# Kernel optimization log

Measured on AMD Instinct MI355X. Metric: run time of the kernel, lower is better.

## Reference

```python
import jax, jax.numpy as jnp
import numpy as np

MODEL_DIM = 1024
EXPAND = 2
INNER = MODEL_DIM * EXPAND      # 2048
STATE = 16
K = 4                           # conv kernel
B, S = 2, 1024


def setup_inputs() -> dict:
    key = jax.random.key(0)
    ks = jax.random.split(key, 12)
    sd = 0.02
    hidden = jax.random.normal(ks[0], (B, S, MODEL_DIM), dtype=jnp.float32)
    w_in = jax.random.normal(ks[1], (2 * INNER, MODEL_DIM), dtype=jnp.float32) * sd
    w_conv = jax.random.normal(ks[2], (INNER, 1, K), dtype=jnp.float32) * 0.2   # depthwise [O, I/g=1, K]
    b_conv = jax.random.normal(ks[3], (INNER,), dtype=jnp.float32) * 0.02
    w_dt = jax.random.normal(ks[4], (INNER, INNER), dtype=jnp.float32) * sd
    b_dt = jnp.full((INNER,), -2.0, dtype=jnp.float32)  # small softplus(dt) at init
    w_b = jax.random.normal(ks[5], (INNER * STATE, INNER), dtype=jnp.float32) * sd
    w_c = jax.random.normal(ks[6], (INNER * STATE, INNER), dtype=jnp.float32) * sd
    w_out = jax.random.normal(ks[7], (MODEL_DIM, INNER), dtype=jnp.float32) * sd
    # a_log = log(arange(1, N+1)) repeated over inner_dim
    a_log = jnp.log(jnp.tile(jnp.arange(1, STATE + 1, dtype=jnp.float32), (INNER, 1)))
    d = jnp.ones((INNER,), dtype=jnp.float32)
    return {"hidden": hidden, "w_in": w_in, "w_conv": w_conv, "b_conv": b_conv,
            "w_dt": w_dt, "b_dt": b_dt, "w_b": w_b, "w_c": w_c, "w_out": w_out,
            "a_log": a_log, "d": d}


def reference(hidden, w_in, w_conv, b_conv, w_dt, b_dt, w_b, w_c, w_out, a_log, d):
    batch, seq_len, _ = hidden.shape
    inner, state_n = a_log.shape
    k = w_conv.shape[-1]

    proj = hidden @ w_in.T                     # [B,S,2*inner]
    u, gate = jnp.split(proj, 2, axis=-1)

    # depthwise causal conv: torch pads k-1 both sides then slices [:, :, :S]
    # which equals left-only padding of k-1
    x = u.transpose(0, 2, 1)                   # [B,inner,S]
    x = jax.lax.conv_general_dilated(
        x, w_conv, window_strides=(1,), padding=[(k - 1, 0)],
        dimension_numbers=("NCH", "OIH", "NCH"), feature_group_count=inner)
    u = jax.nn.silu(x.transpose(0, 2, 1) + b_conv)   # [B,S,inner]
    gate = jax.nn.sigmoid(gate)

    delta = jax.nn.softplus(u @ w_dt.T + b_dt)                       # [B,S,inner]
    bmat = (u @ w_b.T).reshape(batch, seq_len, inner, state_n)       # [B,S,inner,N]
    cmat = (u @ w_c.T).reshape(batch, seq_len, inner, state_n)
    a = -jnp.exp(a_log)                                              # [inner,N]

    def step(state, xs):
        d_t, u_t, b_t, c_t, g_t = xs
        state = jnp.exp(d_t[..., None] * a) * state + d_t[..., None] * b_t * u_t[..., None]
        y = jnp.sum(c_t * state, axis=-1) + d * u_t
        return state, y * g_t

    xs = (delta.transpose(1, 0, 2), u.transpose(1, 0, 2),
          bmat.transpose(1, 0, 2, 3), cmat.transpose(1, 0, 2, 3),
          gate.transpose(1, 0, 2))
    init = jnp.zeros((batch, inner, state_n), dtype=hidden.dtype)
    _, ys = jax.lax.scan(step, init, xs)       # ys: [S,B,inner]
    mixed = ys.transpose(1, 0, 2)              # [B,S,inner]
    return mixed @ w_out.T                     # dropout is identity in eval mode
```

## Files before the change

### kernel.cpp

```cpp
#include <hip/hip_runtime.h>
#include <hip/hip_bf16.h>

typedef __bf16 bf16_t;
typedef __bf16 bf16x8 __attribute__((ext_vector_type(8)));
typedef float f32x4 __attribute__((ext_vector_type(4)));

#define MODEL_DIM 1024
#define INNER 2048
#define STATE 16
#define BATCH 2
#define SEQ 1024
#define BS (BATCH * SEQ)
#define PROJ_N (2 * INNER)
#define BCN (INNER * STATE)
#define NCHUNK 64
#define CLEN (SEQ / NCHUNK)

__device__ __forceinline__ void load_lds_16B(const void* g, void* l) {
  __builtin_amdgcn_global_load_lds(
      (const __attribute__((address_space(1))) unsigned int*)g,
      (__attribute__((address_space(3))) unsigned int*)l,
      16, 0, 0);
}

__global__ void cast_f32_bf16(const float* __restrict__ in,
                              bf16_t* __restrict__ out, long n4) {
  long idx = (long)blockIdx.x * blockDim.x + threadIdx.x;
  long stride = (long)gridDim.x * blockDim.x;
  for (long i = idx; i < n4; i += stride) {
    float4 v = ((const float4*)in)[i];
    union { bf16_t b[4]; ushort4 u; } cv;
    cv.b[0] = (bf16_t)v.x; cv.b[1] = (bf16_t)v.y;
    cv.b[2] = (bf16_t)v.z; cv.b[3] = (bf16_t)v.w;
    ((ushort4*)out)[i] = cv.u;
  }
}

template <int EPI>
__global__ __launch_bounds__(256)
void gemm_bt(const bf16_t* __restrict__ A, const bf16_t* __restrict__ Bt,
             void* __restrict__ C, const float* __restrict__ bias,
             int nbx, int nby, int N, int K) {
  __shared__ bf16_t Ash[128 * 64];
  __shared__ bf16_t Bsh[128 * 64];
  const int tid = threadIdx.x;
  const int wave = tid >> 6, lane = tid & 63;

  const int bid = blockIdx.x;
  const int xcd = bid & 7, local = bid >> 3;
  const int bcol = (xcd * (nbx >> 3) + local / nby) * 128;
  const int brow = (local % nby) * 128;

  const int wr = wave >> 1, wc = wave & 1;

  f32x4 acc[4][4] = {};

  const int seg_base = wave * 4;
  const int lrow = lane >> 3;
  const int scol = ((lane & 7) ^ (lrow & 7)) * 8;
  const int r15 = lane & 15, g = lane >> 4, l7 = lane & 7;

  for (int k0 = 0; k0 < K; k0 += 64) {
#pragma unroll
    for (int c = 0; c < 4; ++c) {
      int seg = seg_base + c;
      int row = seg * 8 + lrow;
      const bf16_t* ga = A + (size_t)(brow + row) * K + k0 + scol;
      load_lds_16B(ga, (void*)(Ash + seg * 512));
      const bf16_t* gb = Bt + (size_t)(bcol + row) * K + k0 + scol;
      load_lds_16B(gb, (void*)(Bsh + seg * 512));
    }
    asm volatile("s_waitcnt vmcnt(0)");
    __syncthreads();

#pragma unroll
    for (int ks = 0; ks < 2; ++ks) {
      bf16x8 af[4], bfr[4];
#pragma unroll
      for (int t = 0; t < 4; ++t) {
        int arow = wr * 64 + t * 16 + r15;
        int brw  = wc * 64 + t * 16 + r15;
        int slot = ((ks * 4 + g) ^ l7) * 8;
        af[t]  = *(const bf16x8*)&Ash[arow * 64 + slot];
        bfr[t] = *(const bf16x8*)&Bsh[brw * 64 + slot];
      }
#pragma unroll
      for (int mt = 0; mt < 4; ++mt)
#pragma unroll
        for (int nt = 0; nt < 4; ++nt)
          acc[mt][nt] = __builtin_amdgcn_mfma_f32_16x16x32_bf16(
              af[mt], bfr[nt], acc[mt][nt], 0, 0, 0);
    }
    __syncthreads();
  }

#pragma unroll
  for (int mt = 0; mt < 4; ++mt) {
#pragma unroll
    for (int nt = 0; nt < 4; ++nt) {
      int col = bcol + wc * 64 + nt * 16 + r15;
#pragma unroll
      for (int j = 0; j < 4; ++j) {
        int row = brow + wr * 64 + mt * 16 + g * 4 + j;
        float v = acc[mt][nt][j];
        size_t idx = (size_t)row * N + col;
        if (EPI == 0) {
          ((float*)C)[idx] = v;
        } else if (EPI == 1) {
          float x = v + bias[col];
          ((float*)C)[idx] = (x > 20.f) ? x : log1pf(__expf(x));
        } else {
          ((bf16_t*)C)[idx] = (bf16_t)v;
        }
      }
    }
  }
}

__global__ __launch_bounds__(256)
void conv_silu(const float* __restrict__ proj, const float* __restrict__ w_conv,
               const float* __restrict__ b_conv, bf16_t* __restrict__ u_bf,
               bf16_t* __restrict__ gate_bf) {
  int idx = blockIdx.x * 256 + threadIdx.x;
  int i = idx & (INNER - 1);
  int s = (idx >> 11) & (SEQ - 1);
  int b = idx >> 21;
  const float* up = proj + (size_t)b * SEQ * PROJ_N + i;
  float w0 = w_conv[i * 4 + 0], w1 = w_conv[i * 4 + 1];
  float w2 = w_conv[i * 4 + 2], w3 = w_conv[i * 4 + 3];
  float acc = b_conv[i];
  acc += up[(size_t)s * PROJ_N] * w3;
  if (s >= 1) acc += up[(size_t)(s - 1) * PROJ_N] * w2;
  if (s >= 2) acc += up[(size_t)(s - 2) * PROJ_N] * w1;
  if (s >= 3) acc += up[(size_t)(s - 3) * PROJ_N] * w0;
  float u = acc / (1.f + __expf(-acc));
  u_bf[idx] = (bf16_t)u;
  float gp = up[(size_t)s * PROJ_N + INNER];
  gate_bf[idx] = (bf16_t)(1.f / (1.f + __expf(-gp)));
}

__global__ __launch_bounds__(256)
void scan_pass1(const float* __restrict__ delta, const bf16_t* __restrict__ u,
                const bf16_t* __restrict__ bmat, const float* __restrict__ a_log,
                float* __restrict__ P, float* __restrict__ E) {
  int t = blockIdx.x * 256 + threadIdx.x;
  int i = t & (INNER - 1);
  int c = (t >> 11) & (NCHUNK - 1);
  int b = t >> 17;
  float an[STATE];
#pragma unroll
  for (int n = 0; n < STATE; ++n) an[n] = -__expf(a_log[i * STATE + n]);
  float st[STATE] = {};
  float dtsum = 0.f;
  size_t base_ch = (size_t)b * SEQ * INNER + i;
  size_t base_bc = (size_t)b * SEQ * BCN + (size_t)i * STATE;
  int s0 = c * CLEN;
  for (int s = s0; s < s0 + CLEN; ++s) {
    float dt = delta[base_ch + (size_t)s * INNER];
    float uv = (float)u[base_ch + (size_t)s * INNER];
    bf16x8 b0 = *(const bf16x8*)&bmat[base_bc + (size_t)s * BCN];
    bf16x8 b1 = *(const bf16x8*)&bmat[base_bc + (size_t)s * BCN + 8];
    float du = dt * uv;
    dtsum += dt;
#pragma unroll
    for (int n = 0; n < 8; ++n)
      st[n] = __expf(dt * an[n]) * st[n] + du * (float)b0[n];
#pragma unroll
    for (int n = 0; n < 8; ++n)
      st[8 + n] = __expf(dt * an[8 + n]) * st[8 + n] + du * (float)b1[n];
  }
  size_t pe = ((size_t)(b * NCHUNK + c) * INNER + i) * STATE;
#pragma unroll
  for (int q = 0; q < 4; ++q) {
    f32x4 vp = {__expf(dtsum * an[q * 4]), __expf(dtsum * an[q * 4 + 1]),
                __expf(dtsum * an[q * 4 + 2]), __expf(dtsum * an[q * 4 + 3])};
    *(f32x4*)&P[pe + q * 4] = vp;
    f32x4 ve = {st[q * 4], st[q * 4 + 1], st[q * 4 + 2], st[q * 4 + 3]};
    *(f32x4*)&E[pe + q * 4] = ve;
  }
}

__global__ __launch_bounds__(256)
void scan_mid(const float* __restrict__ P, float* __restrict__ E) {
  int g = blockIdx.x * 256 + threadIdx.x;
  int n = g & (STATE - 1);
  int i = (g >> 4) & (INNER - 1);
  int b = g >> 15;
  float H = 0.f;
  size_t stride = (size_t)INNER * STATE;
  size_t idx = (size_t)b * NCHUNK * stride + (size_t)i * STATE + n;
  for (int c = 0; c < NCHUNK; ++c) {
    float p = P[idx];
    float e = E[idx];
    E[idx] = H;
    H = p * H + e;
    idx += stride;
  }
}

__global__ __launch_bounds__(256)
void scan_pass2(const float* __restrict__ delta, const bf16_t* __restrict__ u,
                const bf16_t* __restrict__ bmat, const bf16_t* __restrict__ cmat,
                const bf16_t* __restrict__ gate, const float* __restrict__ a_log,
                const float* __restrict__ dvec, const float* __restrict__ E,
                bf16_t* __restrict__ mixed) {
  int t = blockIdx.x * 256 + threadIdx.x;
  int i = t & (INNER - 1);
  int c = (t >> 11) & (NCHUNK - 1);
  int b = t >> 17;
  float an[STATE];
#pragma unroll
  for (int n = 0; n < STATE; ++n) an[n] = -__expf(a_log[i * STATE + n]);
  float st[STATE];
  size_t pe = ((size_t)(b * NCHUNK + c) * INNER + i) * STATE;
#pragma unroll
  for (int q = 0; q < 4; ++q) {
    f32x4 v = *(const f32x4*)&E[pe + q * 4];
    st[q * 4] = v[0]; st[q * 4 + 1] = v[1]; st[q * 4 + 2] = v[2]; st[q * 4 + 3] = v[3];
  }
  float dd = dvec[i];
  size_t base_ch = (size_t)b * SEQ * INNER + i;
  size_t base_bc = (size_t)b * SEQ * BCN + (size_t)i * STATE;
  int s0 = c * CLEN;
  for (int s = s0; s < s0 + CLEN; ++s) {
    float dt = delta[base_ch + (size_t)s * INNER];
    float uv = (float)u[base_ch + (size_t)s * INNER];
    bf16x8 b0 = *(const bf16x8*)&bmat[base_bc + (size_t)s * BCN];
    bf16x8 b1 = *(const bf16x8*)&bmat[base_bc + (size_t)s * BCN + 8];
    bf16x8 c0 = *(const bf16x8*)&cmat[base_bc + (size_t)s * BCN];
    bf16x8 c1 = *(const bf16x8*)&cmat[base_bc + (size_t)s * BCN + 8];
    float du = dt * uv;
    float y = 0.f;
#pragma unroll
    for (int n = 0; n < 8; ++n) {
      st[n] = __expf(dt * an[n]) * st[n] + du * (float)b0[n];
      y += (float)c0[n] * st[n];
    }
#pragma unroll
    for (int n = 0; n < 8; ++n) {
      st[8 + n] = __expf(dt * an[8 + n]) * st[8 + n] + du * (float)b1[n];
      y += (float)c1[n] * st[8 + n];
    }
    float g = (float)gate[base_ch + (size_t)s * INNER];
    mixed[base_ch + (size_t)s * INNER] = (bf16_t)((y + dd * uv) * g);
  }
}

extern "C" void kernel_launch(void* const* d_in, const int* in_sizes, int n_in,
                              void* d_out, int out_size, void* d_ws, size_t ws_size,
                              hipStream_t stream) {
  const float* hidden = (const float*)d_in[0];
  const float* w_in   = (const float*)d_in[1];
  const float* w_conv = (const float*)d_in[2];
  const float* b_conv = (const float*)d_in[3];
  const float* w_dt   = (const float*)d_in[4];
  const float* b_dt   = (const float*)d_in[5];
  const float* w_b    = (const float*)d_in[6];
  const float* w_c    = (const float*)d_in[7];
  const float* w_out  = (const float*)d_in[8];
  const float* a_log  = (const float*)d_in[9];
  const float* dvec   = (const float*)d_in[10];
  float* out = (float*)d_out;

  char* ws = (char*)d_ws;
  bf16_t* hidden_bf = (bf16_t*)ws; ws += (size_t)BS * MODEL_DIM * 2;
  bf16_t* wsmall_bf = (bf16_t*)ws; ws += (size_t)PROJ_N * MODEL_DIM * 2;
  float*  proj      = (float*)ws;  ws += (size_t)BS * PROJ_N * 4;
  bf16_t* u_bf      = (bf16_t*)ws; ws += (size_t)BS * INNER * 2;
  bf16_t* gate_bf   = (bf16_t*)ws; ws += (size_t)BS * INNER * 2;
  float*  delta     = (float*)ws;  ws += (size_t)BS * INNER * 4;
  bf16_t* wbig_bf   = (bf16_t*)ws; ws += (size_t)BCN * INNER * 2;
  bf16_t* bmat      = (bf16_t*)ws; ws += (size_t)BS * BCN * 2;
  bf16_t* cmat      = (bf16_t*)ws; ws += (size_t)BS * BCN * 2;
  bf16_t* mixed     = (bf16_t*)ws; ws += (size_t)BS * INNER * 2;
  float* Pbuf = (float*)wbig_bf;
  float* Ebuf = Pbuf + (size_t)BATCH * NCHUNK * INNER * STATE;

  cast_f32_bf16<<<2048, 256, 0, stream>>>(hidden, hidden_bf, (long)BS * MODEL_DIM / 4);
  cast_f32_bf16<<<2048, 256, 0, stream>>>(w_in, wsmall_bf, (long)PROJ_N * MODEL_DIM / 4);
  gemm_bt<0><<<32 * 16, 256, 0, stream>>>(
      hidden_bf, wsmall_bf, proj, nullptr, 32, 16, PROJ_N, MODEL_DIM);
  conv_silu<<<(BATCH * SEQ * INNER) / 256, 256, 0, stream>>>(proj, w_conv, b_conv, u_bf, gate_bf);
  cast_f32_bf16<<<2048, 256, 0, stream>>>(w_dt, wsmall_bf, (long)INNER * INNER / 4);
  gemm_bt<1><<<16 * 16, 256, 0, stream>>>(
      u_bf, wsmall_bf, delta, b_dt, 16, 16, INNER, INNER);
  cast_f32_bf16<<<2048, 256, 0, stream>>>(w_b, wbig_bf, (long)BCN * INNER / 4);
  gemm_bt<2><<<256 * 16, 256, 0, stream>>>(
      u_bf, wbig_bf, bmat, nullptr, 256, 16, BCN, INNER);
  cast_f32_bf16<<<2048, 256, 0, stream>>>(w_c, wbig_bf, (long)BCN * INNER / 4);
  gemm_bt<2><<<256 * 16, 256, 0, stream>>>(
      u_bf, wbig_bf, cmat, nullptr, 256, 16, BCN, INNER);
  scan_pass1<<<(BATCH * NCHUNK * INNER) / 256, 256, 0, stream>>>(
      delta, u_bf, bmat, a_log, Pbuf, Ebuf);
  scan_mid<<<(BATCH * INNER * STATE) / 256, 256, 0, stream>>>(Pbuf, Ebuf);
  scan_pass2<<<(BATCH * NCHUNK * INNER) / 256, 256, 0, stream>>>(
      delta, u_bf, bmat, cmat, gate_bf, a_log, dvec, Ebuf, mixed);
  cast_f32_bf16<<<2048, 256, 0, stream>>>(w_out, wsmall_bf, (long)MODEL_DIM * INNER / 4);
  gemm_bt<0><<<8 * 16, 256, 0, stream>>>(
      mixed, wsmall_bf, out, nullptr, 8, 16, MODEL_DIM, INNER);
}
```

Baseline: 1.111 ms.

## Add 256x256-tile 8-wave GEMM with double-buffered LDS for B/C projections

Adds gemm_big8, a 512-thread kernel that computes 256x256 output tiles. Each wave holds a 128x64 accumulator slice, with double-buffered LDS, XOR-swizzled layout and direct global-to-LDS loads. Loads for the next k-tile are interleaved across eight MFMA phases, with s_setprio and explicit vmcnt waits. The change targets the two largest GEMMs (B and C projections, N=32768), aiming for more data reuse per tile and better overlap of loads with compute. In exchange it raises register pressure and uses a large LDS footprint, and the grid mapping hardcodes the problem shape.

```diff
diff --git a/kernel.cpp b/kernel.cpp
--- a/kernel.cpp
+++ b/kernel.cpp
@@ -33,6 +33,130 @@
     cv.b[0] = (bf16_t)v.x; cv.b[1] = (bf16_t)v.y;
     cv.b[2] = (bf16_t)v.z; cv.b[3] = (bf16_t)v.w;
     ((ushort4*)out)[i] = cv.u;
+  }
+}
+
+__global__ __launch_bounds__(512, 2)
+void gemm_big8(const bf16_t* __restrict__ Ap, const bf16_t* __restrict__ Bp,
+               bf16_t* __restrict__ C, int N, int K) {
+  __shared__ bf16_t As[2 * 256 * 64];
+  __shared__ bf16_t Bs[2 * 256 * 64];
+  const int tid = threadIdx.x;
+  const int wid = tid >> 6, lane = tid & 63;
+  const int wm = wid >> 2, wn = wid & 3;
+
+  const int bid = blockIdx.x;
+  const int xcd = bid & 7, local = bid >> 3;
+  const int bcol = (xcd * 16 + (local >> 3)) * 256;
+  const int brow = (local & 7) * 256;
+
+  const int lrow = lane >> 3;
+  const int l7 = lane & 7;
+  const int scol = (l7 ^ lrow) * 8;
+  const int r15 = lane & 15, g = lane >> 4;
+
+  const int NT = K >> 6, NI = NT >> 1;
+
+  f32x4 acc[8][4] = {};
+
+#define FENCE() asm volatile("" ::: "memory")
+
+#define STAGE_A(BUF, T, H)                                                    \
+  {                                                                           \
+    _Pragma("unroll") for (int j = 0; j < 2; ++j) {                           \
+      const int rs = j * 128 + (H) * 64;                                      \
+      load_lds_16B(Ap + (size_t)(brow + rs + wid * 8 + lrow) * K +            \
+                       (size_t)(T) * 64 + scol,                               \
+                   (void*)(As + (BUF) * 16384 + rs * 64 + wid * 512));        \
+    }                                                                         \
+  }
+#define STAGE_B(BUF, T, H)                                                    \
+  {                                                                           \
+    _Pragma("unroll") for (int j = 0; j < 2; ++j) {                           \
+      const int rs = (2 * j + (wid >> 2)) * 64 + (H) * 32 + (wid & 3) * 8;    \
+      load_lds_16B(Bp + (size_t)(bcol + rs + lrow) * K +                      \
+                       (size_t)(T) * 64 + scol,                               \
+                   (void*)(Bs + (BUF) * 16384 + rs * 64));                    \
+    }                                                                         \
+  }
+
+#define PHASE(BUF, MH, NH, STAGE_CODE, VMN)                                   \
+  {                                                                           \
+    bf16x8 af[4][2], bv[2][2];                                                \
+    _Pragma("unroll") for (int m = 0; m < 4; ++m) {                           \
+      int arow = wm * 128 + (MH) * 64 + m * 16 + r15;                         \
+      _Pragma("unroll") for (int ks = 0; ks < 2; ++ks)                        \
+        af[m][ks] = *(const bf16x8*)&As[(BUF) * 16384 + arow * 64 +           \
+                                        (((ks * 4 + g) ^ l7) * 8)];           \
+    }                                                                         \
+    _Pragma("unroll") for (int n = 0; n < 2; ++n) {                           \
+      int brw = wn * 64 + (NH) * 32 + n * 16 + r15;                           \
+      _Pragma("unroll") for (int ks = 0; ks < 2; ++ks)                        \
+        bv[n][ks] = *(const bf16x8*)&Bs[(BUF) * 16384 + brw * 64 +            \
+                                        (((ks * 4 + g) ^ l7) * 8)];           \
+    }                                                                         \
+    STAGE_CODE;                                                               \
+    FENCE();                                                                  \
+    __builtin_amdgcn_s_barrier();                                             \
+    FENCE();                                                                  \
+    __builtin_amdgcn_s_setprio(1);                                            \
+    _Pragma("unroll") for (int ks = 0; ks < 2; ++ks)                          \
+      _Pragma("unroll") for (int m = 0; m < 4; ++m)                           \
+        _Pragma("unroll") for (int n = 0; n < 2; ++n)                         \
+          acc[(MH) * 4 + m][(NH) * 2 + n] =                                   \
+              __builtin_amdgcn_mfma_f32_16x16x32_bf16(                        \
+                  af[m][ks], bv[n][ks], acc[(MH) * 4 + m][(NH) * 2 + n],      \
+                  0, 0, 0);                                                   \
+    __builtin_amdgcn_s_setprio(0);                                            \
+    asm volatile("s_waitcnt vmcnt(" #VMN ")" ::: "memory");                   \
+    __builtin_amdgcn_s_barrier();                                             \
+    FENCE();                                                                  \
+  }
+
+  STAGE_A(0, 0, 0); STAGE_A(0, 0, 1); STAGE_B(0, 0, 0); STAGE_B(0, 0, 1);
+  STAGE_A(1, 1, 0); STAGE_B(1, 1, 0);
+  asm volatile("s_waitcnt vmcnt(4)" ::: "memory");
+  __builtin_amdgcn_s_barrier();
+  FENCE();
+
+  for (int i = 0; i < NI - 1; ++i) {
+    const int t1 = 2 * i + 1, t2 = 2 * i + 2, t3 = 2 * i + 3;
+    PHASE(0, 0, 0, STAGE_B(1, t1, 1), 8);
+    PHASE(0, 0, 1, STAGE_A(1, t1, 1), 8);
+    PHASE(0, 1, 0, STAGE_A(0, t2, 0), 8);
+    PHASE(0, 1, 1, STAGE_B(0, t2, 0), 8);
+    PHASE(1, 0, 0, STAGE_B(0, t2, 1), 8);
+    PHASE(1, 0, 1, STAGE_A(0, t2, 1), 8);
+    PHASE(1, 1, 0, STAGE_A(1, t3, 0), 8);
+    PHASE(1, 1, 1, STAGE_B(1, t3, 0), 8);
+  }
+  {
+    const int tl = NT - 1;
+    PHASE(0, 0, 0, STAGE_B(1, tl, 1), 8);
+    PHASE(0, 0, 1, STAGE_A(1, tl, 1), 8);
+    PHASE(0, 1, 0, , 8);
+    PHASE(0, 1, 1, , 4);
+    PHASE(1, 0, 0, , 2);
+    PHASE(1, 0, 1, , 0);
+    PHASE(1, 1, 0, , 0);
+    PHASE(1, 1, 1, , 0);
+  }
+#undef PHASE
+#undef STAGE_A
+#undef STAGE_B
+#undef FENCE
+
+#pragma unroll
+  for (int mf = 0; mf < 8; ++mf) {
+#pragma unroll
+    for (int nf = 0; nf < 4; ++nf) {
+      int col = bcol + wn * 64 + nf * 16 + r15;
+#pragma unroll
+      for (int j = 0; j < 4; ++j) {
+        int row = brow + wm * 128 + mf * 16 + g * 4 + j;
+        C[(size_t)row * N + col] = (bf16_t)acc[mf][nf][j];
+      }
+    }
   }
 }
 
@@ -182,10 +306,10 @@
 
 __global__ __launch_bounds__(256)
 void scan_mid(const float* __restrict__ P, float* __restrict__ E) {
-  int g = blockIdx.x * 256 + threadIdx.x;
-  int n = g & (STATE - 1);
-  int i = (g >> 4) & (INNER - 1);
-  int b = g >> 15;
+  int gi = blockIdx.x * 256 + threadIdx.x;
+  int n = gi & (STATE - 1);
+  int i = (gi >> 4) & (INNER - 1);
+  int b = gi >> 15;
   float H = 0.f;
   size_t stride = (size_t)INNER * STATE;
   size_t idx = (size_t)b * NCHUNK * stride + (size_t)i * STATE + n;
@@ -285,11 +409,9 @@
   gemm_bt<1><<<16 * 16, 256, 0, stream>>>(
       u_bf, wsmall_bf, delta, b_dt, 16, 16, INNER, INNER);
   cast_f32_bf16<<<2048, 256, 0, stream>>>(w_b, wbig_bf, (long)BCN * INNER / 4);
-  gemm_bt<2><<<256 * 16, 256, 0, stream>>>(
-      u_bf, wbig_bf, bmat, nullptr, 256, 16, BCN, INNER);
+  gemm_big8<<<1024, 512, 0, stream>>>(u_bf, wbig_bf, bmat, BCN, INNER);
   cast_f32_bf16<<<2048, 256, 0, stream>>>(w_c, wbig_bf, (long)BCN * INNER / 4);
-  gemm_bt<2><<<256 * 16, 256, 0, stream>>>(
-      u_bf, wbig_bf, cmat, nullptr, 256, 16, BCN, INNER);
+  gemm_big8<<<1024, 512, 0, stream>>>(u_bf, wbig_bf, cmat, BCN, INNER);
   scan_pass1<<<(BATCH * NCHUNK * INNER) / 256, 256, 0, stream>>>(
       delta, u_bf, bmat, a_log, Pbuf, Ebuf);
   scan_mid<<<(BATCH * INNER * STATE) / 256, 256, 0, stream>>>(Pbuf, Ebuf);
```

Result: slower. 1.192 ms (+7.2%).
